# Kernel tuning notes

Measured on AMD Instinct MI355X. Metric: run time of the kernel, lower is better.

The kernel has to match this reference:

```python
import jax, jax.numpy as jnp
import numpy as np

DT = 0.001  # fixed dt in SimplifiedSSM.forward
LN_EPS = 1e-5


def _layernorm(x, g, b):
    m = jnp.mean(x, axis=-1, keepdims=True)
    v = jnp.mean(jnp.square(x - m), axis=-1, keepdims=True)
    return (x - m) * jax.lax.rsqrt(v + LN_EPS) * g + b


def setup_inputs() -> dict:
    key = jax.random.key(0)
    ks = jax.random.split(key, 12)
    Bn, C, H, W = 8, 1024, 32, 32
    depth, S = 4, 128
    d = C
    inp = {
        "x": jax.random.normal(ks[0], (Bn, C, H, W), dtype=jnp.float32),
        # SSM params, stacked over depth. A scaled by 0.1 for numerical stability
        # of the length-1024 recurrence (same math, tamer eigenvalues).
        "A": 0.1 * jax.random.normal(ks[1], (depth, S, S), dtype=jnp.float32),
        "Bp": jax.random.normal(ks[2], (depth, S, d), dtype=jnp.float32),
        "Cp": jax.random.normal(ks[3], (depth, d, S), dtype=jnp.float32),
        "Dp": jax.random.normal(ks[4], (depth, d), dtype=jnp.float32),
        # Linear layers (PyTorch convention: y = x @ W.T + b)
        "Wi": jax.random.normal(ks[5], (depth, d, d), dtype=jnp.float32) / np.sqrt(d),
        "bi": jax.random.normal(ks[6], (depth, d), dtype=jnp.float32) * 0.01,
        "Wo": jax.random.normal(ks[7], (depth, d, d), dtype=jnp.float32) / np.sqrt(d),
        "bo": jax.random.normal(ks[8], (depth, d), dtype=jnp.float32) * 0.01,
        # LayerNorm affine params
        "gamma": jnp.ones((depth, d), dtype=jnp.float32),
        "beta": jnp.zeros((depth, d), dtype=jnp.float32),
    }
    return inp


def reference(x, A, Bp, Cp, Dp, Wi, bi, Wo, bo, gamma, beta):
    Bn, C, H, W = x.shape
    depth, S, _ = A.shape
    # b c h w -> b (h w) c
    seq = x.reshape(Bn, C, H * W).transpose(0, 2, 1)
    eye = jnp.eye(S, dtype=x.dtype)
    for i in range(depth):
        n = _layernorm(seq, gamma[i], beta[i])
        u = n @ Wi[i].T + bi[i]                       # (B, L, d)
        A_bar = eye + DT * A[i]                       # (S, S)
        ub = jnp.einsum('bld,sd->lbs', u, DT * Bp[i]) # (L, B, S)

        def step(h, ub_t):
            h = h @ A_bar.T + ub_t
            return h, h

        h0 = jnp.zeros((Bn, S), dtype=x.dtype)
        _, hs = jax.lax.scan(step, h0, ub)            # hs: (L, B, S)
        y = jnp.einsum('lbs,ds->bld', hs, Cp[i]) + u * Dp[i]
        seq = seq + y @ Wo[i].T + bo[i]
    return seq.transpose(0, 2, 1).reshape(Bn, C, H, W)
```

## Files before the change

kernel.cpp:

```cpp
#include <hip/hip_runtime.h>
#include <stdint.h>

#define DT_STEP 0.001f
#define LN_EPS  1e-5f
#define Bn      8
#define Lseq    1024
#define Dm      1024
#define Sn      128
#define DEPTH   4
#define Mrows   (Bn * Lseq)
#define Qc      32
#define NCHUNK  (Lseq / Qc)
#define NPOW    33

typedef short bf16x8 __attribute__((ext_vector_type(8)));
typedef float f32x4  __attribute__((ext_vector_type(4)));

__device__ __forceinline__ unsigned short f2bf(float f) {
    unsigned int u = __float_as_uint(f);
    u += 0x7fffu + ((u >> 16) & 1u);
    return (unsigned short)(u >> 16);
}

#define GLOAD_LDS16(gp, lp)                                                \
    __builtin_amdgcn_global_load_lds(                                      \
        (const __attribute__((address_space(1))) unsigned int*)(gp),       \
        (__attribute__((address_space(3))) unsigned int*)(lp), 16, 0, 0)

__global__ __launch_bounds__(256) void prep_conv(const float* __restrict__ Wo,
                                                 const float* __restrict__ Dp,
                                                 const float* __restrict__ Bp,
                                                 unsigned short* __restrict__ Woh,
                                                 unsigned short* __restrict__ Wo2h,
                                                 unsigned short* __restrict__ Bph) {
    int z = blockIdx.y;
    int bx = blockIdx.x;
    if (bx < 1024) {
        int i = (bx * 256 + threadIdx.x) * 4;
        const float* S = Wo + (size_t)z * Dm * Dm;
        float4 v = *(const float4*)(S + i);
        int c = i & (Dm - 1);
        float4 d = *(const float4*)(Dp + (size_t)z * Dm + c);
        ushort4 o1, o2;
        o1.x = f2bf(v.x); o1.y = f2bf(v.y); o1.z = f2bf(v.z); o1.w = f2bf(v.w);
        o2.x = f2bf(v.x * d.x); o2.y = f2bf(v.y * d.y);
        o2.z = f2bf(v.z * d.z); o2.w = f2bf(v.w * d.w);
        *(ushort4*)(Woh  + (size_t)z * Dm * Dm + i) = o1;
        *(ushort4*)(Wo2h + (size_t)z * Dm * Dm + i) = o2;
    } else {
        int i = ((bx - 1024) * 256 + threadIdx.x) * 4;
        float4 v = *(const float4*)(Bp + (size_t)z * Sn * Dm + i);
        ushort4 o;
        o.x = f2bf(v.x); o.y = f2bf(v.y); o.z = f2bf(v.z); o.w = f2bf(v.w);
        *(ushort4*)(Bph + (size_t)z * Sn * Dm + i) = o;
    }
}

__global__ __launch_bounds__(256) void transpose_f2bf(const float* __restrict__ src,
                                                      unsigned short* __restrict__ dst,
                                                      int R, int C) {
    __shared__ float t[32][33];
    int z = blockIdx.z;
    const float* S = src + (size_t)z * R * C;
    unsigned short* D = dst + (size_t)z * R * C;
    int r0 = blockIdx.y * 32, c0 = blockIdx.x * 32;
    int tx = threadIdx.x & 31, ty = threadIdx.x >> 5;
    for (int rr = ty; rr < 32; rr += 8)
        t[rr][tx] = S[(size_t)(r0 + rr) * C + c0 + tx];
    __syncthreads();
    for (int rr = ty; rr < 32; rr += 8)
        D[(size_t)(c0 + rr) * R + r0 + tx] = f2bf(t[tx][rr]);
}

__global__ __launch_bounds__(256) void c2dt_boeff(const float* __restrict__ Bp,
                                                  const float* __restrict__ bi,
                                                  const float* __restrict__ Wo,
                                                  const float* __restrict__ Dp,
                                                  const float* __restrict__ bo,
                                                  float* __restrict__ c2dt,
                                                  float* __restrict__ boeff) {
    int z = blockIdx.x, j = blockIdx.y;
    int tid = threadIdx.x;
    float acc;
    if (j < Sn) {
        const float* br = Bp + ((size_t)z * Sn + j) * Dm;
        const float* bb = bi + (size_t)z * Dm;
        float4 v = *(const float4*)(br + tid * 4);
        float4 w = *(const float4*)(bb + tid * 4);
        acc = v.x * w.x + v.y * w.y + v.z * w.z + v.w * w.w;
    } else {
        int c = j - Sn;
        const float* wr = Wo + ((size_t)z * Dm + c) * Dm;
        const float* dp = Dp + (size_t)z * Dm;
        const float* bb = bi + (size_t)z * Dm;
        float4 w = *(const float4*)(wr + tid * 4);
        float4 d = *(const float4*)(dp + tid * 4);
        float4 b = *(const float4*)(bb + tid * 4);
        acc = w.x * d.x * b.x + w.y * d.y * b.y + w.z * d.z * b.z + w.w * d.w * b.w;
    }
#pragma unroll
    for (int off = 32; off > 0; off >>= 1) acc += __shfl_down(acc, off, 64);
    __shared__ float red[4];
    if ((tid & 63) == 0) red[tid >> 6] = acc;
    __syncthreads();
    if (tid == 0) {
        float tot = red[0] + red[1] + red[2] + red[3];
        if (j < Sn) c2dt[z * Sn + j] = DT_STEP * tot;
        else        boeff[(size_t)z * Dm + (j - Sn)] = bo[(size_t)z * Dm + (j - Sn)] + tot;
    }
}

__global__ __launch_bounds__(1024) void transpose_bll(const float* __restrict__ src,
                                                      float* __restrict__ dst) {
    __shared__ float tile[32][33];
    int b  = blockIdx.z;
    int i0 = blockIdx.y * 32, j0 = blockIdx.x * 32;
    int tx = threadIdx.x, ty = threadIdx.y;
    const float* S = src + (size_t)b * Dm * Lseq;
    float*       D = dst + (size_t)b * Dm * Lseq;
    tile[ty][tx] = S[(size_t)(j0 + ty) * 1024 + i0 + tx];
    __syncthreads();
    D[(size_t)(i0 + ty) * 1024 + j0 + tx] = tile[tx][ty];
}

__global__ __launch_bounds__(256) void ln_kernel(const float* __restrict__ x,
                                                 unsigned short* __restrict__ outp,
                                                 const float* __restrict__ g,
                                                 const float* __restrict__ bta) {
    int row = blockIdx.x;
    int tid = threadIdx.x;
    const float* xr = x + (size_t)row * Dm;
    float4 v = *(const float4*)(xr + tid * 4);
    float s  = v.x + v.y + v.z + v.w;
    float ss = v.x * v.x + v.y * v.y + v.z * v.z + v.w * v.w;
#pragma unroll
    for (int off = 32; off > 0; off >>= 1) {
        s  += __shfl_down(s, off, 64);
        ss += __shfl_down(ss, off, 64);
    }
    __shared__ float red[8];
    __shared__ float mv[2];
    int wave = tid >> 6, lane = tid & 63;
    if (lane == 0) { red[wave] = s; red[4 + wave] = ss; }
    __syncthreads();
    if (tid == 0) {
        float st  = red[0] + red[1] + red[2] + red[3];
        float sst = red[4] + red[5] + red[6] + red[7];
        float mean = st / (float)Dm;
        float var  = sst / (float)Dm - mean * mean;
        mv[0] = mean;
        mv[1] = rsqrtf(var + LN_EPS);
    }
    __syncthreads();
    float mean = mv[0], rstd = mv[1];
    int c = tid * 4;
    float4 gv = *(const float4*)(g + c);
    float4 bv = *(const float4*)(bta + c);
    ushort4 o;
    o.x = f2bf((v.x - mean) * rstd * gv.x + bv.x);
    o.y = f2bf((v.y - mean) * rstd * gv.y + bv.y);
    o.z = f2bf((v.z - mean) * rstd * gv.z + bv.z);
    o.w = f2bf((v.w - mean) * rstd * gv.w + bv.w);
    *(ushort4*)(outp + (size_t)row * Dm + c) = o;
}

__global__ __launch_bounds__(512) void gemm_ub(
    const unsigned short* __restrict__ A,
    const unsigned short* __restrict__ B,
    float* __restrict__ ub,
    const float* __restrict__ c2dtL) {
    __shared__ __align__(16) unsigned short As[256 * 8];
    __shared__ __align__(16) unsigned short Bs[1024 * 8];
    int row0 = blockIdx.x * 32;
    int tid  = threadIdx.x;
    int wave = tid >> 6, lane = tid & 63;
    int wn = wave * 16;
    int lr = lane & 15, lq = lane >> 4;

    int rowA = tid >> 3;
    int kclA = (tid & 7) ^ ((tid >> 3) & 7);
    int rowS[2], kclS[2], slotOff[2];
#pragma unroll
    for (int q = 0; q < 2; q++) {
        int s = tid + q * 512;
        rowS[q] = s >> 3;
        kclS[q] = (s & 7) ^ ((s >> 3) & 7);
        slotOff[q] = s * 8;
    }
    int aoff[2][2], boff[2];
#pragma unroll
    for (int i = 0; i < 2; i++)
#pragma unroll
        for (int h = 0; h < 2; h++) {
            int ra = i * 16 + lr;
            aoff[i][h] = (ra * 8 + ((lq + 4 * h) ^ (ra & 7))) * 8;
        }
#pragma unroll
    for (int h = 0; h < 2; h++) {
        int rn = wn + lr;
        boff[h] = (rn * 8 + ((lq + 4 * h) ^ (rn & 7))) * 8;
    }

    f32x4 acc[2];
#pragma unroll
    for (int i = 0; i < 2; i++) acc[i] = (f32x4){0.f, 0.f, 0.f, 0.f};

    for (int k0 = 0; k0 < Dm; k0 += 64) {
        const unsigned short* Abr = A + (size_t)row0 * Dm + k0;
        const unsigned short* Bbr = B + k0;
        __syncthreads();
        if (tid < 256)
            GLOAD_LDS16(Abr + (size_t)rowA * Dm + kclA * 8, &As[tid * 8]);
#pragma unroll
        for (int q = 0; q < 2; q++)
            GLOAD_LDS16(Bbr + (size_t)rowS[q] * Dm + kclS[q] * 8, &Bs[slotOff[q]]);
        __syncthreads();
#pragma unroll
        for (int h = 0; h < 2; h++) {
            bf16x8 af[2], bfr;
#pragma unroll
            for (int i = 0; i < 2; i++) af[i] = *(const bf16x8*)&As[aoff[i][h]];
            bfr = *(const bf16x8*)&Bs[boff[h]];
#pragma unroll
            for (int i = 0; i < 2; i++)
                acc[i] = __builtin_amdgcn_mfma_f32_16x16x32_bf16(af[i], bfr,
                                                                 acc[i], 0, 0, 0);
        }
    }
#pragma unroll
    for (int i = 0; i < 2; i++)
#pragma unroll
        for (int r = 0; r < 4; r++) {
            int row = row0 + i * 16 + lq * 4 + r;
            int col = wn + lr;
            ub[(size_t)row * Sn + col] = acc[i][r] + c2dtL[col];
        }
}

__device__ __forceinline__ void gemm64_body(
    int flat, unsigned short* As, unsigned short* Bs,
    const unsigned short* __restrict__ A, const unsigned short* __restrict__ B,
    float* __restrict__ C, const float* __restrict__ bias, int K) {
    int rb = flat & 63, cb = flat >> 6;
    int row0 = rb * 128, col0 = cb * 64;
    int tid  = threadIdx.x;
    int wave = tid >> 6, lane = tid & 63;
    int wm = (wave & 1) * 64, wn = (wave >> 1) * 16;
    int lr = lane & 15, lq = lane >> 4;

    int rowS[2], kclS[2], slotOff[2];
#pragma unroll
    for (int q = 0; q < 2; q++) {
        int s = tid + q * 512;
        rowS[q] = s >> 3;
        kclS[q] = (s & 7) ^ ((s >> 3) & 7);
        slotOff[q] = s * 8;
    }
    int rowB = tid >> 3;
    int kclB = (tid & 7) ^ ((tid >> 3) & 7);

    int aoff[4][2], boff[2];
#pragma unroll
    for (int i = 0; i < 4; i++)
#pragma unroll
        for (int h = 0; h < 2; h++) {
            int ra = wm + i * 16 + lr;
            aoff[i][h] = (ra * 8 + ((lq + 4 * h) ^ (ra & 7))) * 8;
        }
#pragma unroll
    for (int h = 0; h < 2; h++) {
        int rn = wn + lr;
        boff[h] = (rn * 8 + ((lq + 4 * h) ^ (rn & 7))) * 8;
    }

    f32x4 acc[4];
#pragma unroll
    for (int i = 0; i < 4; i++) acc[i] = (f32x4){0.f, 0.f, 0.f, 0.f};

    for (int k0 = 0; k0 < K; k0 += 64) {
        const unsigned short* Abr = A + (size_t)row0 * K + k0;
        const unsigned short* Bbr = B + (size_t)col0 * K + k0;
        __syncthreads();
#pragma unroll
        for (int q = 0; q < 2; q++)
            GLOAD_LDS16(Abr + (size_t)rowS[q] * K + kclS[q] * 8, &As[slotOff[q]]);
        GLOAD_LDS16(Bbr + (size_t)rowB * K + kclB * 8, &Bs[tid * 8]);
        __syncthreads();
#pragma unroll
        for (int h = 0; h < 2; h++) {
            bf16x8 af[4], bf;
#pragma unroll
            for (int i = 0; i < 4; i++) af[i] = *(const bf16x8*)&As[aoff[i][h]];
            bf = *(const bf16x8*)&Bs[boff[h]];
#pragma unroll
            for (int i = 0; i < 4; i++)
                acc[i] = __builtin_amdgcn_mfma_f32_16x16x32_bf16(af[i], bf,
                                                                 acc[i], 0, 0, 0);
        }
    }
#pragma unroll
    for (int i = 0; i < 4; i++)
#pragma unroll
        for (int r = 0; r < 4; r++) {
            int row = row0 + wm + i * 16 + lq * 4 + r;
            int col = col0 + wn + lr;
            size_t idx = (size_t)row * Dm + col;
            float v = acc[i][r];
            if (bias) v += bias[col];
            C[idx] = C[idx] + v;
        }
}

__global__ __launch_bounds__(512) void gemm_w3k(const unsigned short* __restrict__ hs_bf,
                                                const unsigned short* __restrict__ W3,
                                                float* __restrict__ seq) {
    __shared__ __align__(16) unsigned short As[1024 * 8];
    __shared__ __align__(16) unsigned short Bs[512 * 8];
    gemm64_body(blockIdx.x, As, Bs, hs_bf, W3, seq, nullptr, Sn);
}

__global__ __launch_bounds__(512) void mega_scan_w4(
    const unsigned short* __restrict__ nbuf,
    const unsigned short* __restrict__ W4,
    float* __restrict__ seq,
    const float* __restrict__ boeff,
    const float* __restrict__ ub,
    float* __restrict__ hs,
    const float* __restrict__ Abar) {
    __shared__ __align__(16) unsigned short As[1024 * 8];
    __shared__ __align__(16) unsigned short Bs[512 * 8];
    __shared__ __align__(16) float hsh[Sn];
    __shared__ __align__(16) float hp[4][Sn];
    int tid = threadIdx.x;

    if (blockIdx.x >= 256) {
        gemm64_body(blockIdx.x - 256, As, Bs, nbuf, W4, seq, boeff, Dm);
        return;
    }

    int chunk = blockIdx.x;
    int b = chunk >> 5;
    int c = chunk & 31;
    int s = tid & 127, kq = tid >> 7;
    float arow[32];
#pragma unroll
    for (int j = 0; j < 32; j += 4) {
        float4 v = *(const float4*)(Abar + (size_t)s * Sn + kq * 32 + j);
        arow[j] = v.x; arow[j + 1] = v.y; arow[j + 2] = v.z; arow[j + 3] = v.w;
    }
    if (tid < 128) hsh[tid] = 0.f;
    __syncthreads();
    size_t base = (size_t)(b * Lseq + c * Qc) * Sn + s;
    float ut = (kq == 0) ? ub[base] : 0.f;
    const float* hq = &hsh[kq * 32];
    for (int t = 0; t < Qc; t++) {
        float utn = (kq == 0 && t + 1 < Qc) ? ub[base + (size_t)(t + 1) * Sn] : 0.f;
        float a0 = 0.f, a1 = 0.f, a2 = 0.f, a3 = 0.f;
#pragma unroll
        for (int j = 0; j < 32; j += 16) {
            float4 h0 = *(const float4*)&hq[j];
            float4 h1 = *(const float4*)&hq[j + 4];
            float4 h2 = *(const float4*)&hq[j + 8];
            float4 h3 = *(const float4*)&hq[j + 12];
            a0 += arow[j + 0] * h0.x + arow[j + 1] * h0.y + arow[j + 2] * h0.z + arow[j + 3] * h0.w;
            a1 += arow[j + 4] * h1.x + arow[j + 5] * h1.y + arow[j + 6] * h1.z + arow[j + 7] * h1.w;
            a2 += arow[j + 8] * h2.x + arow[j + 9] * h2.y + arow[j + 10] * h2.z + arow[j + 11] * h2.w;
            a3 += arow[j + 12] * h3.x + arow[j + 13] * h3.y + arow[j + 14] * h3.z + arow[j + 15] * h3.w;
        }
        hp[kq][s] = (a0 + a1) + (a2 + a3);
        __syncthreads();
        if (kq == 0) {
            float hv = ut + (hp[0][s] + hp[1][s]) + (hp[2][s] + hp[3][s]);
            hs[base + (size_t)t * Sn] = hv;
            hsh[s] = hv;
        }
        __syncthreads();
        ut = utn;
    }
}

__global__ __launch_bounds__(512) void gemm_bk64(
    const unsigned short* __restrict__ A1, int sA1,
    const unsigned short* __restrict__ B1, int sB1,
    unsigned short* __restrict__ Ch,
    int ny, int N, int K, float scale,
    long batchA, long batchB, long batchC) {
    __shared__ __align__(16) unsigned short As[1024 * 8];
    __shared__ __align__(16) unsigned short Bs[1024 * 8];
    int flat = blockIdx.x;
    int rb = flat % ny, cb = flat / ny;
    int row0 = rb * 128, col0 = cb * 128;
    int z = blockIdx.y;
    int tid  = threadIdx.x;
    int wave = tid >> 6, lane = tid & 63;
    int wm = (wave & 1) * 64, wn = (wave >> 1) * 32;
    int lr = lane & 15, lq = lane >> 4;

    int rowS[2], kclS[2], slotOff[2];
#pragma unroll
    for (int q = 0; q < 2; q++) {
        int s = tid + q * 512;
        rowS[q] = s >> 3;
        kclS[q] = (s & 7) ^ ((s >> 3) & 7);
        slotOff[q] = s * 8;
    }
    int aoff[4][2], boff[2][2];
#pragma unroll
    for (int i = 0; i < 4; i++)
#pragma unroll
        for (int h = 0; h < 2; h++) {
            int ra = wm + i * 16 + lr;
            aoff[i][h] = (ra * 8 + ((lq + 4 * h) ^ (ra & 7))) * 8;
        }
#pragma unroll
    for (int j = 0; j < 2; j++)
#pragma unroll
        for (int h = 0; h < 2; h++) {
            int rn = wn + j * 16 + lr;
            boff[j][h] = (rn * 8 + ((lq + 4 * h) ^ (rn & 7))) * 8;
        }

    const unsigned short* Ab = A1 + (size_t)z * batchA;
    const unsigned short* Bb = B1 + (size_t)z * batchB + (size_t)col0 * sB1;

    f32x4 acc[4][2];
#pragma unroll
    for (int i = 0; i < 4; i++)
#pragma unroll
        for (int j = 0; j < 2; j++) acc[i][j] = (f32x4){0.f, 0.f, 0.f, 0.f};

    for (int k0 = 0; k0 < K; k0 += 64) {
        const unsigned short* Abr = Ab + (size_t)row0 * sA1 + k0;
        const unsigned short* Bbr = Bb + k0;
        __syncthreads();
#pragma unroll
        for (int q = 0; q < 2; q++) {
            GLOAD_LDS16(Abr + (size_t)rowS[q] * sA1 + kclS[q] * 8, &As[slotOff[q]]);
            GLOAD_LDS16(Bbr + (size_t)rowS[q] * sB1 + kclS[q] * 8, &Bs[slotOff[q]]);
        }
        __syncthreads();
#pragma unroll
        for (int h = 0; h < 2; h++) {
            bf16x8 af[4], bfr[2];
#pragma unroll
            for (int i = 0; i < 4; i++) af[i]  = *(const bf16x8*)&As[aoff[i][h]];
#pragma unroll
            for (int j = 0; j < 2; j++) bfr[j] = *(const bf16x8*)&Bs[boff[j][h]];
#pragma unroll
            for (int i = 0; i < 4; i++)
#pragma unroll
                for (int j = 0; j < 2; j++)
                    acc[i][j] = __builtin_amdgcn_mfma_f32_16x16x32_bf16(af[i], bfr[j],
                                                                       acc[i][j], 0, 0, 0);
        }
    }
#pragma unroll
    for (int i = 0; i < 4; i++)
#pragma unroll
        for (int j = 0; j < 2; j++)
#pragma unroll
            for (int r = 0; r < 4; r++) {
                int row = row0 + wm + i * 16 + lq * 4 + r;
                int col = col0 + wn + j * 16 + lr;
                Ch[(size_t)z * batchC + (size_t)row * N + col] = f2bf(acc[i][j][r] * scale);
            }
}

__global__ __launch_bounds__(128) void pow_init(const float* __restrict__ Amat,
                                                float* __restrict__ Pow) {
    int i = blockIdx.x;
    int s = blockIdx.y;
    int k = threadIdx.x;
    float eye = (s == k) ? 1.f : 0.f;
    size_t base = (size_t)i * NPOW * (Sn * Sn);
    Pow[base + (size_t)s * Sn + k] = eye;
    Pow[base + (size_t)(Sn * Sn) + (size_t)s * Sn + k] =
        eye + DT_STEP * Amat[(size_t)i * Sn * Sn + (size_t)s * Sn + k];
}

__global__ __launch_bounds__(256) void pow_mul(float* __restrict__ Pow, int m, int kmax) {
    int job = blockIdx.z;
    int i  = job / kmax;
    int kk = job % kmax + 1;
    const float* Pa = Pow + ((size_t)i * NPOW + m) * (Sn * Sn);
    const float* Pb = Pow + ((size_t)i * NPOW + kk) * (Sn * Sn);
    float*       Pc = Pow + ((size_t)i * NPOW + m + kk) * (Sn * Sn);
    int r0 = blockIdx.y * 64, c0 = blockIdx.x * 32;
    __shared__ float Asl[64 * 129];
    __shared__ float Bsl[128 * 32];
    int tx = threadIdx.x, ty = threadIdx.y;
    int tid = ty * 16 + tx;
    for (int idx = tid; idx < 64 * 128; idx += 256) {
        int r = idx >> 7, cc = idx & 127;
        Asl[r * 129 + cc] = Pa[(size_t)(r0 + r) * 128 + cc];
    }
    for (int idx = tid; idx < 128 * 32; idx += 256) {
        int r = idx >> 5, cc = idx & 31;
        Bsl[r * 32 + cc] = Pb[(size_t)r * 128 + c0 + cc];
    }
    __syncthreads();
    float acc[4][2] = {{0.f,0.f},{0.f,0.f},{0.f,0.f},{0.f,0.f}};
    for (int k = 0; k < 128; k++) {
        float b0 = Bsl[k * 32 + tx * 2];
        float b1 = Bsl[k * 32 + tx * 2 + 1];
#pragma unroll
        for (int r = 0; r < 4; r++) {
            float a = Asl[(ty * 4 + r) * 129 + k];
            acc[r][0] += a * b0;
            acc[r][1] += a * b1;
        }
    }
#pragma unroll
    for (int r = 0; r < 4; r++) {
        Pc[(size_t)(r0 + ty * 4 + r) * 128 + c0 + tx * 2]     = acc[r][0];
        Pc[(size_t)(r0 + ty * 4 + r) * 128 + c0 + tx * 2 + 1] = acc[r][1];
    }
}

__global__ __launch_bounds__(128) void carry_scan(const float* __restrict__ hs,
                                                  const float* __restrict__ AQ,
                                                  float* __restrict__ carry) {
    int b = blockIdx.x;
    int s = threadIdx.x;
    float le[NCHUNK];
#pragma unroll
    for (int c = 0; c < NCHUNK; c++)
        le[c] = hs[(size_t)(b * Lseq + c * Qc + Qc - 1) * Sn + s];
    float arow[Sn];
#pragma unroll
    for (int k = 0; k < Sn; k += 4) {
        float4 v = *(const float4*)(AQ + (size_t)s * Sn + k);
        arow[k] = v.x; arow[k + 1] = v.y; arow[k + 2] = v.z; arow[k + 3] = v.w;
    }
    __shared__ __align__(16) float csh[Sn];
    csh[s] = 0.f;
    __syncthreads();
    for (int c = 0; c < NCHUNK; c++) {
        carry[((size_t)b * NCHUNK + c) * Sn + s] = csh[s];
        float a0 = 0.f, a1 = 0.f, a2 = 0.f, a3 = 0.f;
#pragma unroll
        for (int k = 0; k < Sn; k += 16) {
            float4 h0 = *(const float4*)&csh[k];
            float4 h1 = *(const float4*)&csh[k + 4];
            float4 h2 = *(const float4*)&csh[k + 8];
            float4 h3 = *(const float4*)&csh[k + 12];
            a0 += arow[k + 0] * h0.x + arow[k + 1] * h0.y + arow[k + 2] * h0.z + arow[k + 3] * h0.w;
            a1 += arow[k + 4] * h1.x + arow[k + 5] * h1.y + arow[k + 6] * h1.z + arow[k + 7] * h1.w;
            a2 += arow[k + 8] * h2.x + arow[k + 9] * h2.y + arow[k + 10] * h2.z + arow[k + 11] * h2.w;
            a3 += arow[k + 12] * h3.x + arow[k + 13] * h3.y + arow[k + 14] * h3.z + arow[k + 15] * h3.w;
        }
        float cv = le[c] + (a0 + a1) + (a2 + a3);
        __syncthreads();
        csh[s] = cv;
        __syncthreads();
    }
}

__global__ __launch_bounds__(256) void fixup_scan(const float* __restrict__ hs,
                                                  unsigned short* __restrict__ hs_bf,
                                                  const float* __restrict__ PowLayer,
                                                  const float* __restrict__ carry) {
    int t  = blockIdx.x;
    int c4 = blockIdx.y;
    const float* P = PowLayer + (size_t)(t + 1) * (Sn * Sn);
    __shared__ float Pl[Sn * 65];
    __shared__ float cl[4][Bn * Sn];
    int tid = threadIdx.x;
#pragma unroll
    for (int cc = 0; cc < 4; cc++)
        for (int idx = tid; idx < Bn * Sn; idx += 256)
            cl[cc][idx] = carry[((size_t)(idx >> 7) * NCHUNK + (c4 * 4 + cc)) * Sn + (idx & 127)];
    int s = tid & 127, bh = tid >> 7;
    float acc[4][4];
#pragma unroll
    for (int cc = 0; cc < 4; cc++)
#pragma unroll
        for (int j = 0; j < 4; j++) acc[cc][j] = 0.f;
    for (int kh = 0; kh < 2; kh++) {
        __syncthreads();
        for (int idx = tid; idx < Sn * 64; idx += 256) {
            int r = idx >> 6, kk = idx & 63;
            Pl[r * 65 + kk] = P[(size_t)r * Sn + kh * 64 + kk];
        }
        __syncthreads();
        for (int kk = 0; kk < 64; kk++) {
            float pw = Pl[s * 65 + kk];
            int kg = kh * 64 + kk;
#pragma unroll
            for (int cc = 0; cc < 4; cc++)
#pragma unroll
                for (int j = 0; j < 4; j++)
                    acc[cc][j] += pw * cl[cc][(bh * 4 + j) * Sn + kg];
        }
    }
#pragma unroll
    for (int cc = 0; cc < 4; cc++) {
        int c = c4 * 4 + cc;
#pragma unroll
        for (int j = 0; j < 4; j++) {
            int bb = bh * 4 + j;
            size_t rowi = (size_t)(bb * Lseq + c * Qc + t) * Sn + s;
            hs_bf[rowi] = f2bf(hs[rowi] + acc[cc][j]);
        }
    }
}

extern "C" void kernel_launch(void* const* d_in, const int* in_sizes, int n_in,
                              void* d_out, int out_size, void* d_ws, size_t ws_size,
                              hipStream_t stream) {
    const float* x     = (const float*)d_in[0];
    const float* Am    = (const float*)d_in[1];
    const float* Bp    = (const float*)d_in[2];
    const float* Cp    = (const float*)d_in[3];
    const float* Dp    = (const float*)d_in[4];
    const float* Wi    = (const float*)d_in[5];
    const float* bi    = (const float*)d_in[6];
    const float* Wo    = (const float*)d_in[7];
    const float* bo    = (const float*)d_in[8];
    const float* gamma = (const float*)d_in[9];
    const float* beta  = (const float*)d_in[10];
    float* out = (float*)d_out;
    (void)in_sizes; (void)n_in; (void)out_size; (void)ws_size;

    char* ws = (char*)d_ws;
    float*          seq   = (float*)(ws + (size_t)0);
    unsigned short* nbuf  = (unsigned short*)(ws + (size_t)33554432);
    unsigned short* WiTh  = (unsigned short*)(ws + (size_t)33554432);
    unsigned short* Woh   = (unsigned short*)(ws + (size_t)41943040);
    unsigned short* W4h   = (unsigned short*)(ws + (size_t)50331648);
    float*          boeff = (float*)(ws + (size_t)58720256);
    float*          ub    = (float*)(ws + (size_t)67108864);
    float*          hs    = (float*)(ws + (size_t)71303168);
    unsigned short* hs_bf = (unsigned short*)(ws + (size_t)75497472);
    float*          Pow   = (float*)(ws + (size_t)77594624);
    float*          carry = (float*)(ws + (size_t)86245376);
    unsigned short* Wo2h  = (unsigned short*)(ws + (size_t)94765056);
    unsigned short* Bph   = (unsigned short*)(ws + (size_t)103153664);
    unsigned short* CpTh  = (unsigned short*)(ws + (size_t)104202240);
    unsigned short* M2h   = (unsigned short*)(ws + (size_t)105250816);
    unsigned short* W3h   = (unsigned short*)(ws + (size_t)106299392);
    float*          c2dt  = (float*)(ws + (size_t)107347968);

    const long WW = (long)Dm * Dm;
    const long SW = (long)Sn * Dm;

    hipLaunchKernelGGL(prep_conv, dim3(1024 + 128, DEPTH), dim3(256), 0, stream,
                       Wo, Dp, Bp, Woh, Wo2h, Bph);
    hipLaunchKernelGGL(transpose_f2bf, dim3(32, 32, DEPTH), dim3(256), 0, stream,
                       Wi, WiTh, Dm, Dm);
    hipLaunchKernelGGL(transpose_f2bf, dim3(4, 32, DEPTH), dim3(256), 0, stream,
                       Cp, CpTh, Dm, Sn);
    hipLaunchKernelGGL(c2dt_boeff, dim3(DEPTH, Sn + Dm), dim3(256), 0, stream,
                       Bp, bi, Wo, Dp, bo, c2dt, boeff);

    hipLaunchKernelGGL(gemm_bk64, dim3(8, DEPTH), dim3(512), 0, stream,
                       Bph, Dm, WiTh, Dm, M2h, 1, Dm, Dm, DT_STEP, SW, WW, SW);
    hipLaunchKernelGGL(gemm_bk64, dim3(8, DEPTH), dim3(512), 0, stream,
                       Woh, Dm, CpTh, Dm, W3h, 8, Sn, Dm, 1.f, WW, SW, SW);
    hipLaunchKernelGGL(gemm_bk64, dim3(8 * 8, DEPTH), dim3(512), 0, stream,
                       Wo2h, Dm, WiTh, Dm, W4h, 8, Dm, Dm, 1.f, WW, WW, WW);

    hipLaunchKernelGGL(transpose_bll, dim3(32, 32, Bn), dim3(32, 32), 0, stream, x, seq);

    hipLaunchKernelGGL(pow_init, dim3(DEPTH, Sn), dim3(Sn), 0, stream, Am, Pow);
    for (int m = 1; m < Qc; m <<= 1) {
        hipLaunchKernelGGL(pow_mul, dim3(4, 2, DEPTH * m), dim3(16, 16), 0, stream,
                           Pow, m, m);
    }

    for (int i = 0; i < DEPTH; i++) {
        const unsigned short* M2_i = M2h + (size_t)i * SW;
        const unsigned short* W3_i = W3h + (size_t)i * SW;
        const unsigned short* W4_i = W4h + (size_t)i * WW;
        const float* PowL = Pow + (size_t)i * NPOW * (Sn * Sn);

        hipLaunchKernelGGL(ln_kernel, dim3(Mrows), dim3(256), 0, stream,
                           seq, nbuf, gamma + i * Dm, beta + i * Dm);
        hipLaunchKernelGGL(gemm_ub, dim3(Mrows / 32), dim3(512), 0, stream,
                           nbuf, M2_i, ub, c2dt + i * Sn);
        hipLaunchKernelGGL(mega_scan_w4, dim3(256 + 1024), dim3(512), 0, stream,
                           nbuf, W4_i, seq, boeff + i * Dm,
                           ub, hs, PowL + (size_t)Sn * Sn);
        hipLaunchKernelGGL(carry_scan, dim3(Bn), dim3(Sn), 0, stream,
                           hs, PowL + (size_t)Qc * Sn * Sn, carry);
        hipLaunchKernelGGL(fixup_scan, dim3(Qc, NCHUNK / 4), dim3(256), 0, stream,
                           hs, hs_bf, PowL, carry);
        hipLaunchKernelGGL(gemm_w3k, dim3(1024), dim3(512), 0, stream,
                           hs_bf, W3_i, seq);
    }

    hipLaunchKernelGGL(transpose_bll, dim3(32, 32, Bn), dim3(32, 32), 0, stream, seq, out);
}
```

Before: 740.4 us.

## Fuse LayerNorm into ub GEMM and spread W4 GEMM across scan phases

LayerNorm is computed inside the ub GEMM kernel, with each block normalizing its 32 rows, writing them to nbuf and then running the GEMM, so one launch is removed. The chunk scan, carry scan and fixup scan become modes of one kernel, and the W4 output GEMM tiles are split across these three launches (512, 256 and 256 tiles) so the serial scan blocks run alongside GEMM work. The aim is to hide the low-occupancy scan phases, especially the 8-block carry scan, behind useful GEMM work. The risks are that the ub GEMM grid is now only 256 blocks with a serial LN prologue per block, and that the fixup work is spread across more threads, each carrying fewer accumulators.

```diff
diff --git a/kernel.cpp b/kernel.cpp
--- a/kernel.cpp
+++ b/kernel.cpp
@@ -123,56 +123,68 @@
     D[(size_t)(i0 + ty) * 1024 + j0 + tx] = tile[tx][ty];
 }
 
-__global__ __launch_bounds__(256) void ln_kernel(const float* __restrict__ x,
-                                                 unsigned short* __restrict__ outp,
-                                                 const float* __restrict__ g,
-                                                 const float* __restrict__ bta) {
-    int row = blockIdx.x;
-    int tid = threadIdx.x;
-    const float* xr = x + (size_t)row * Dm;
-    float4 v = *(const float4*)(xr + tid * 4);
-    float s  = v.x + v.y + v.z + v.w;
-    float ss = v.x * v.x + v.y * v.y + v.z * v.z + v.w * v.w;
-#pragma unroll
-    for (int off = 32; off > 0; off >>= 1) {
-        s  += __shfl_down(s, off, 64);
-        ss += __shfl_down(ss, off, 64);
-    }
-    __shared__ float red[8];
-    __shared__ float mv[2];
-    int wave = tid >> 6, lane = tid & 63;
-    if (lane == 0) { red[wave] = s; red[4 + wave] = ss; }
-    __syncthreads();
-    if (tid == 0) {
-        float st  = red[0] + red[1] + red[2] + red[3];
-        float sst = red[4] + red[5] + red[6] + red[7];
-        float mean = st / (float)Dm;
-        float var  = sst / (float)Dm - mean * mean;
-        mv[0] = mean;
-        mv[1] = rsqrtf(var + LN_EPS);
-    }
-    __syncthreads();
-    float mean = mv[0], rstd = mv[1];
-    int c = tid * 4;
-    float4 gv = *(const float4*)(g + c);
-    float4 bv = *(const float4*)(bta + c);
-    ushort4 o;
-    o.x = f2bf((v.x - mean) * rstd * gv.x + bv.x);
-    o.y = f2bf((v.y - mean) * rstd * gv.y + bv.y);
-    o.z = f2bf((v.z - mean) * rstd * gv.z + bv.z);
-    o.w = f2bf((v.w - mean) * rstd * gv.w + bv.w);
-    *(ushort4*)(outp + (size_t)row * Dm + c) = o;
-}
-
-__global__ __launch_bounds__(512) void gemm_ub(
-    const unsigned short* __restrict__ A,
-    const unsigned short* __restrict__ B,
+__global__ __launch_bounds__(512) void ln_ub(
+    const float* __restrict__ seq,
+    unsigned short* __restrict__ nbuf,
+    const unsigned short* __restrict__ M2,
     float* __restrict__ ub,
+    const float* __restrict__ gam,
+    const float* __restrict__ bet,
     const float* __restrict__ c2dtL) {
     __shared__ __align__(16) unsigned short As[256 * 8];
     __shared__ __align__(16) unsigned short Bs[1024 * 8];
+    __shared__ float mrow[32], rrow[32];
     int row0 = blockIdx.x * 32;
-    int tid  = threadIdx.x;
+    int tid = threadIdx.x;
+
+    {
+        int r = tid >> 4, l = tid & 15;
+        const float* xr = seq + (size_t)(row0 + r) * Dm + l * 4;
+        float s = 0.f, ss = 0.f;
+#pragma unroll
+        for (int j = 0; j < 16; j++) {
+            float4 v = *(const float4*)(xr + j * 64);
+            s  += v.x + v.y + v.z + v.w;
+            ss += v.x * v.x + v.y * v.y + v.z * v.z + v.w * v.w;
+        }
+        s += __shfl_xor(s, 1, 16);  ss += __shfl_xor(ss, 1, 16);
+        s += __shfl_xor(s, 2, 16);  ss += __shfl_xor(ss, 2, 16);
+        s += __shfl_xor(s, 4, 16);  ss += __shfl_xor(ss, 4, 16);
+        s += __shfl_xor(s, 8, 16);  ss += __shfl_xor(ss, 8, 16);
+        if (l == 0) {
+            float mean = s / (float)Dm;
+            float var  = ss / (float)Dm - mean * mean;
+            mrow[r] = mean;
+            rrow[r] = rsqrtf(var + LN_EPS);
+        }
+    }
+    __syncthreads();
+#pragma unroll
+    for (int g = 0; g < 8; g++) {
+        int gi = tid + g * 512;
+        int rA = gi >> 7, gc = gi & 127;
+        int col = gc * 8;
+        const float* p = seq + (size_t)(row0 + rA) * Dm + col;
+        float4 v0 = *(const float4*)(p);
+        float4 v1 = *(const float4*)(p + 4);
+        float m = mrow[rA], rs = rrow[rA];
+        float4 g0 = *(const float4*)(gam + col);
+        float4 g1 = *(const float4*)(gam + col + 4);
+        float4 b0 = *(const float4*)(bet + col);
+        float4 b1 = *(const float4*)(bet + col + 4);
+        bf16x8 pk;
+        pk[0] = (short)f2bf((v0.x - m) * rs * g0.x + b0.x);
+        pk[1] = (short)f2bf((v0.y - m) * rs * g0.y + b0.y);
+        pk[2] = (short)f2bf((v0.z - m) * rs * g0.z + b0.z);
+        pk[3] = (short)f2bf((v0.w - m) * rs * g0.w + b0.w);
+        pk[4] = (short)f2bf((v1.x - m) * rs * g1.x + b1.x);
+        pk[5] = (short)f2bf((v1.y - m) * rs * g1.y + b1.y);
+        pk[6] = (short)f2bf((v1.z - m) * rs * g1.z + b1.z);
+        pk[7] = (short)f2bf((v1.w - m) * rs * g1.w + b1.w);
+        *(bf16x8*)(nbuf + (size_t)(row0 + rA) * Dm + col) = pk;
+    }
+    __syncthreads();
+
     int wave = tid >> 6, lane = tid & 63;
     int wn = wave * 16;
     int lr = lane & 15, lq = lane >> 4;
@@ -206,8 +218,8 @@
     for (int i = 0; i < 2; i++) acc[i] = (f32x4){0.f, 0.f, 0.f, 0.f};
 
     for (int k0 = 0; k0 < Dm; k0 += 64) {
-        const unsigned short* Abr = A + (size_t)row0 * Dm + k0;
-        const unsigned short* Bbr = B + k0;
+        const unsigned short* Abr = nbuf + (size_t)row0 * Dm + k0;
+        const unsigned short* Bbr = M2 + k0;
         __syncthreads();
         if (tid < 256)
             GLOAD_LDS16(Abr + (size_t)rowA * Dm + kclA * 8, &As[tid * 8]);
@@ -319,63 +331,151 @@
     gemm64_body(blockIdx.x, As, Bs, hs_bf, W3, seq, nullptr, Sn);
 }
 
-__global__ __launch_bounds__(512) void mega_scan_w4(
+__global__ __launch_bounds__(512) void mega2(
+    int mode, int nserial, int gemmFlat0,
     const unsigned short* __restrict__ nbuf,
     const unsigned short* __restrict__ W4,
     float* __restrict__ seq,
     const float* __restrict__ boeff,
     const float* __restrict__ ub,
     float* __restrict__ hs,
-    const float* __restrict__ Abar) {
-    __shared__ __align__(16) unsigned short As[1024 * 8];
-    __shared__ __align__(16) unsigned short Bs[512 * 8];
-    __shared__ __align__(16) float hsh[Sn];
-    __shared__ __align__(16) float hp[4][Sn];
+    unsigned short* __restrict__ hs_bf,
+    const float* __restrict__ PowL,
+    float* __restrict__ carryb) {
+    __shared__ __align__(16) char smem[33280];
     int tid = threadIdx.x;
 
-    if (blockIdx.x >= 256) {
-        gemm64_body(blockIdx.x - 256, As, Bs, nbuf, W4, seq, boeff, Dm);
+    if ((int)blockIdx.x >= nserial) {
+        unsigned short* As = (unsigned short*)smem;
+        unsigned short* Bs = (unsigned short*)(smem + 16384);
+        gemm64_body(gemmFlat0 + (int)blockIdx.x - nserial, As, Bs,
+                    nbuf, W4, seq, boeff, Dm);
         return;
     }
 
-    int chunk = blockIdx.x;
-    int b = chunk >> 5;
-    int c = chunk & 31;
-    int s = tid & 127, kq = tid >> 7;
-    float arow[32];
-#pragma unroll
-    for (int j = 0; j < 32; j += 4) {
-        float4 v = *(const float4*)(Abar + (size_t)s * Sn + kq * 32 + j);
-        arow[j] = v.x; arow[j + 1] = v.y; arow[j + 2] = v.z; arow[j + 3] = v.w;
-    }
-    if (tid < 128) hsh[tid] = 0.f;
-    __syncthreads();
-    size_t base = (size_t)(b * Lseq + c * Qc) * Sn + s;
-    float ut = (kq == 0) ? ub[base] : 0.f;
-    const float* hq = &hsh[kq * 32];
-    for (int t = 0; t < Qc; t++) {
-        float utn = (kq == 0 && t + 1 < Qc) ? ub[base + (size_t)(t + 1) * Sn] : 0.f;
-        float a0 = 0.f, a1 = 0.f, a2 = 0.f, a3 = 0.f;
-#pragma unroll
-        for (int j = 0; j < 32; j += 16) {
-            float4 h0 = *(const float4*)&hq[j];
-            float4 h1 = *(const float4*)&hq[j + 4];
-            float4 h2 = *(const float4*)&hq[j + 8];
-            float4 h3 = *(const float4*)&hq[j + 12];
-            a0 += arow[j + 0] * h0.x + arow[j + 1] * h0.y + arow[j + 2] * h0.z + arow[j + 3] * h0.w;
-            a1 += arow[j + 4] * h1.x + arow[j + 5] * h1.y + arow[j + 6] * h1.z + arow[j + 7] * h1.w;
-            a2 += arow[j + 8] * h2.x + arow[j + 9] * h2.y + arow[j + 10] * h2.z + arow[j + 11] * h2.w;
-            a3 += arow[j + 12] * h3.x + arow[j + 13] * h3.y + arow[j + 14] * h3.z + arow[j + 15] * h3.w;
-        }
-        hp[kq][s] = (a0 + a1) + (a2 + a3);
+    if (mode == 0) {
+        float* hsh = (float*)smem;
+        float* hp  = hsh + 128;
+        int chunk = blockIdx.x;
+        int b = chunk >> 5, c = chunk & 31;
+        int s = tid & 127, kq = tid >> 7;
+        const float* Abar = PowL + (size_t)Sn * Sn;
+        float arow[32];
+#pragma unroll
+        for (int j = 0; j < 32; j += 4) {
+            float4 v = *(const float4*)(Abar + (size_t)s * Sn + kq * 32 + j);
+            arow[j] = v.x; arow[j + 1] = v.y; arow[j + 2] = v.z; arow[j + 3] = v.w;
+        }
+        if (tid < 128) hsh[tid] = 0.f;
         __syncthreads();
-        if (kq == 0) {
-            float hv = ut + (hp[0][s] + hp[1][s]) + (hp[2][s] + hp[3][s]);
-            hs[base + (size_t)t * Sn] = hv;
-            hsh[s] = hv;
-        }
+        size_t base = (size_t)(b * Lseq + c * Qc) * Sn + s;
+        float ut = (kq == 0) ? ub[base] : 0.f;
+        const float* hq = &hsh[kq * 32];
+        for (int t = 0; t < Qc; t++) {
+            float utn = (kq == 0 && t + 1 < Qc) ? ub[base + (size_t)(t + 1) * Sn] : 0.f;
+            float a0 = 0.f, a1 = 0.f, a2 = 0.f, a3 = 0.f;
+#pragma unroll
+            for (int j = 0; j < 32; j += 16) {
+                float4 h0 = *(const float4*)&hq[j];
+                float4 h1 = *(const float4*)&hq[j + 4];
+                float4 h2 = *(const float4*)&hq[j + 8];
+                float4 h3 = *(const float4*)&hq[j + 12];
+                a0 += arow[j + 0] * h0.x + arow[j + 1] * h0.y + arow[j + 2] * h0.z + arow[j + 3] * h0.w;
+                a1 += arow[j + 4] * h1.x + arow[j + 5] * h1.y + arow[j + 6] * h1.z + arow[j + 7] * h1.w;
+                a2 += arow[j + 8] * h2.x + arow[j + 9] * h2.y + arow[j + 10] * h2.z + arow[j + 11] * h2.w;
+                a3 += arow[j + 12] * h3.x + arow[j + 13] * h3.y + arow[j + 14] * h3.z + arow[j + 15] * h3.w;
+            }
+            hp[kq * 128 + s] = (a0 + a1) + (a2 + a3);
+            __syncthreads();
+            if (kq == 0) {
+                float hv = ut + (hp[s] + hp[128 + s]) + (hp[256 + s] + hp[384 + s]);
+                hs[base + (size_t)t * Sn] = hv;
+                hsh[s] = hv;
+            }
+            __syncthreads();
+            ut = utn;
+        }
+    } else if (mode == 1) {
+        float* csh = (float*)smem;
+        float* cp  = csh + 128;
+        int b = blockIdx.x;
+        int s = tid & 127, kq = tid >> 7;
+        const float* AQ = PowL + (size_t)Qc * Sn * Sn;
+        float arow[32];
+#pragma unroll
+        for (int j = 0; j < 32; j += 4) {
+            float4 v = *(const float4*)(AQ + (size_t)s * Sn + kq * 32 + j);
+            arow[j] = v.x; arow[j + 1] = v.y; arow[j + 2] = v.z; arow[j + 3] = v.w;
+        }
+        if (tid < 128) csh[tid] = 0.f;
         __syncthreads();
-        ut = utn;
+        float len = (kq == 0) ? hs[(size_t)(b * Lseq + Qc - 1) * Sn + s] : 0.f;
+        const float* cq = &csh[kq * 32];
+        for (int c = 0; c < NCHUNK; c++) {
+            float le_c = len;
+            len = (kq == 0 && c + 1 < NCHUNK)
+                    ? hs[(size_t)(b * Lseq + (c + 1) * Qc + Qc - 1) * Sn + s] : 0.f;
+            if (kq == 0) carryb[((size_t)b * NCHUNK + c) * Sn + s] = csh[s];
+            float a0 = 0.f, a1 = 0.f, a2 = 0.f, a3 = 0.f;
+#pragma unroll
+            for (int j = 0; j < 32; j += 16) {
+                float4 h0 = *(const float4*)&cq[j];
+                float4 h1 = *(const float4*)&cq[j + 4];
+                float4 h2 = *(const float4*)&cq[j + 8];
+                float4 h3 = *(const float4*)&cq[j + 12];
+                a0 += arow[j + 0] * h0.x + arow[j + 1] * h0.y + arow[j + 2] * h0.z + arow[j + 3] * h0.w;
+                a1 += arow[j + 4] * h1.x + arow[j + 5] * h1.y + arow[j + 6] * h1.z + arow[j + 7] * h1.w;
+                a2 += arow[j + 8] * h2.x + arow[j + 9] * h2.y + arow[j + 10] * h2.z + arow[j + 11] * h2.w;
+                a3 += arow[j + 12] * h3.x + arow[j + 13] * h3.y + arow[j + 14] * h3.z + arow[j + 15] * h3.w;
+            }
+            cp[kq * 128 + s] = (a0 + a1) + (a2 + a3);
+            __syncthreads();
+            if (kq == 0)
+                csh[s] = le_c + (cp[s] + cp[128 + s]) + (cp[256 + s] + cp[384 + s]);
+            __syncthreads();
+        }
+    } else {
+        float* Pl = (float*)smem;
+        float* cl = (float*)(smem + 16896);
+        int ser = blockIdx.x;
+        int t = ser & 31, c4 = ser >> 5;
+        const float* P = PowL + (size_t)(t + 1) * (Sn * Sn);
+#pragma unroll
+        for (int cc = 0; cc < 4; cc++)
+            for (int idx = tid; idx < Bn * Sn; idx += 512)
+                cl[cc * 1024 + idx] =
+                    carryb[((size_t)(idx >> 7) * NCHUNK + (c4 * 4 + cc)) * Sn + (idx & 127)];
+        int s = tid & 127, bh = tid >> 7;
+        float acc[4][2];
+#pragma unroll
+        for (int cc = 0; cc < 4; cc++) { acc[cc][0] = 0.f; acc[cc][1] = 0.f; }
+        for (int kh = 0; kh < 4; kh++) {
+            __syncthreads();
+            for (int idx = tid; idx < Sn * 32; idx += 512) {
+                int r = idx >> 5, kk = idx & 31;
+                Pl[r * 33 + kk] = P[(size_t)r * Sn + kh * 32 + kk];
+            }
+            __syncthreads();
+            for (int kk = 0; kk < 32; kk++) {
+                float pw = Pl[s * 33 + kk];
+                int kg = kh * 32 + kk;
+#pragma unroll
+                for (int cc = 0; cc < 4; cc++)
+#pragma unroll
+                    for (int j = 0; j < 2; j++)
+                        acc[cc][j] += pw * cl[cc * 1024 + (bh * 2 + j) * Sn + kg];
+            }
+        }
+#pragma unroll
+        for (int cc = 0; cc < 4; cc++) {
+            int c = c4 * 4 + cc;
+#pragma unroll
+            for (int j = 0; j < 2; j++) {
+                int bb = bh * 2 + j;
+                size_t rowi = (size_t)(bb * Lseq + c * Qc + t) * Sn + s;
+                hs_bf[rowi] = f2bf(hs[rowi] + acc[cc][j]);
+            }
+        }
     }
 }
 
@@ -514,94 +614,6 @@
     for (int r = 0; r < 4; r++) {
         Pc[(size_t)(r0 + ty * 4 + r) * 128 + c0 + tx * 2]     = acc[r][0];
         Pc[(size_t)(r0 + ty * 4 + r) * 128 + c0 + tx * 2 + 1] = acc[r][1];
-    }
-}
-
-__global__ __launch_bounds__(128) void carry_scan(const float* __restrict__ hs,
-                                                  const float* __restrict__ AQ,
-                                                  float* __restrict__ carry) {
-    int b = blockIdx.x;
-    int s = threadIdx.x;
-    float le[NCHUNK];
-#pragma unroll
-    for (int c = 0; c < NCHUNK; c++)
-        le[c] = hs[(size_t)(b * Lseq + c * Qc + Qc - 1) * Sn + s];
-    float arow[Sn];
-#pragma unroll
-    for (int k = 0; k < Sn; k += 4) {
-        float4 v = *(const float4*)(AQ + (size_t)s * Sn + k);
-        arow[k] = v.x; arow[k + 1] = v.y; arow[k + 2] = v.z; arow[k + 3] = v.w;
-    }
-    __shared__ __align__(16) float csh[Sn];
-    csh[s] = 0.f;
-    __syncthreads();
-    for (int c = 0; c < NCHUNK; c++) {
-        carry[((size_t)b * NCHUNK + c) * Sn + s] = csh[s];
-        float a0 = 0.f, a1 = 0.f, a2 = 0.f, a3 = 0.f;
-#pragma unroll
-        for (int k = 0; k < Sn; k += 16) {
-            float4 h0 = *(const float4*)&csh[k];
-            float4 h1 = *(const float4*)&csh[k + 4];
-            float4 h2 = *(const float4*)&csh[k + 8];
-            float4 h3 = *(const float4*)&csh[k + 12];
-            a0 += arow[k + 0] * h0.x + arow[k + 1] * h0.y + arow[k + 2] * h0.z + arow[k + 3] * h0.w;
-            a1 += arow[k + 4] * h1.x + arow[k + 5] * h1.y + arow[k + 6] * h1.z + arow[k + 7] * h1.w;
-            a2 += arow[k + 8] * h2.x + arow[k + 9] * h2.y + arow[k + 10] * h2.z + arow[k + 11] * h2.w;
-            a3 += arow[k + 12] * h3.x + arow[k + 13] * h3.y + arow[k + 14] * h3.z + arow[k + 15] * h3.w;
-        }
-        float cv = le[c] + (a0 + a1) + (a2 + a3);
-        __syncthreads();
-        csh[s] = cv;
-        __syncthreads();
-    }
-}
-
-__global__ __launch_bounds__(256) void fixup_scan(const float* __restrict__ hs,
-                                                  unsigned short* __restrict__ hs_bf,
-                                                  const float* __restrict__ PowLayer,
-                                                  const float* __restrict__ carry) {
-    int t  = blockIdx.x;
-    int c4 = blockIdx.y;
-    const float* P = PowLayer + (size_t)(t + 1) * (Sn * Sn);
-    __shared__ float Pl[Sn * 65];
-    __shared__ float cl[4][Bn * Sn];
-    int tid = threadIdx.x;
-#pragma unroll
-    for (int cc = 0; cc < 4; cc++)
-        for (int idx = tid; idx < Bn * Sn; idx += 256)
-            cl[cc][idx] = carry[((size_t)(idx >> 7) * NCHUNK + (c4 * 4 + cc)) * Sn + (idx & 127)];
-    int s = tid & 127, bh = tid >> 7;
-    float acc[4][4];
-#pragma unroll
-    for (int cc = 0; cc < 4; cc++)
-#pragma unroll
-        for (int j = 0; j < 4; j++) acc[cc][j] = 0.f;
-    for (int kh = 0; kh < 2; kh++) {
-        __syncthreads();
-        for (int idx = tid; idx < Sn * 64; idx += 256) {
-            int r = idx >> 6, kk = idx & 63;
-            Pl[r * 65 + kk] = P[(size_t)r * Sn + kh * 64 + kk];
-        }
-        __syncthreads();
-        for (int kk = 0; kk < 64; kk++) {
-            float pw = Pl[s * 65 + kk];
-            int kg = kh * 64 + kk;
-#pragma unroll
-            for (int cc = 0; cc < 4; cc++)
-#pragma unroll
-                for (int j = 0; j < 4; j++)
-                    acc[cc][j] += pw * cl[cc][(bh * 4 + j) * Sn + kg];
-        }
-    }
-#pragma unroll
-    for (int cc = 0; cc < 4; cc++) {
-        int c = c4 * 4 + cc;
-#pragma unroll
-        for (int j = 0; j < 4; j++) {
-            int bb = bh * 4 + j;
-            size_t rowi = (size_t)(bb * Lseq + c * Qc + t) * Sn + s;
-            hs_bf[rowi] = f2bf(hs[rowi] + acc[cc][j]);
-        }
     }
 }
 
@@ -674,17 +686,18 @@
         const unsigned short* W4_i = W4h + (size_t)i * WW;
         const float* PowL = Pow + (size_t)i * NPOW * (Sn * Sn);
 
-        hipLaunchKernelGGL(ln_kernel, dim3(Mrows), dim3(256), 0, stream,
-                           seq, nbuf, gamma + i * Dm, beta + i * Dm);
-        hipLaunchKernelGGL(gemm_ub, dim3(Mrows / 32), dim3(512), 0, stream,
-                           nbuf, M2_i, ub, c2dt + i * Sn);
-        hipLaunchKernelGGL(mega_scan_w4, dim3(256 + 1024), dim3(512), 0, stream,
-                           nbuf, W4_i, seq, boeff + i * Dm,
-                           ub, hs, PowL + (size_t)Sn * Sn);
-        hipLaunchKernelGGL(carry_scan, dim3(Bn), dim3(Sn), 0, stream,
-                           hs, PowL + (size_t)Qc * Sn * Sn, carry);
-        hipLaunchKernelGGL(fixup_scan, dim3(Qc, NCHUNK / 4), dim3(256), 0, stream,
-                           hs, hs_bf, PowL, carry);
+        hipLaunchKernelGGL(ln_ub, dim3(256), dim3(512), 0, stream,
+                           seq, nbuf, M2_i, ub, gamma + i * Dm, beta + i * Dm,
+                           c2dt + i * Sn);
+        hipLaunchKernelGGL(mega2, dim3(256 + 512), dim3(512), 0, stream,
+                           0, 256, 0, nbuf, W4_i, seq, boeff + i * Dm,
+                           ub, hs, hs_bf, PowL, carry);
+        hipLaunchKernelGGL(mega2, dim3(8 + 256), dim3(512), 0, stream,
+                           1, 8, 512, nbuf, W4_i, seq, boeff + i * Dm,
+                           ub, hs, hs_bf, PowL, carry);
+        hipLaunchKernelGGL(mega2, dim3(256 + 256), dim3(512), 0, stream,
+                           2, 256, 768, nbuf, W4_i, seq, boeff + i * Dm,
+                           ub, hs, hs_bf, PowL, carry);
         hipLaunchKernelGGL(gemm_w3k, dim3(1024), dim3(512), 0, stream,
                            hs_bf, W3_i, seq);
     }
```

Measured after the change: 715.6 us. -3.3%, faster.
